# Optimization experiments

Measured on AMD Instinct MI355X. Metric: run time of the kernel, lower is better.

The kernel has to match this reference:

```python
import jax, jax.numpy as jnp
import numpy as np

B, F, T, K = 131072, 1024, 100, 32  # batch, num_features, num_trees, features per tree (sqrt(F))


def setup_inputs() -> dict:
    key = jax.random.key(0)
    kx, kw = jax.random.split(key)
    x = jax.random.normal(kx, (B, F), dtype=jnp.float32)
    # per-tree random feature selection without replacement (np.random.choice replace=False)
    rng = np.random.default_rng(0)
    idx = np.argsort(rng.random((T, F)), axis=1)[:, :K].astype(np.int32)
    feature_indices = jnp.asarray(idx)
    feature_thresholds = jnp.zeros((T, K), dtype=jnp.float32)  # lazy-init zeros in original
    feature_weights = jax.random.uniform(kw, (T, K), dtype=jnp.float32)  # torch.rand
    return {
        "x": x,
        "feature_indices": feature_indices,
        "feature_thresholds": feature_thresholds,
        "feature_weights": feature_weights,
    }


def reference(x, feature_indices, feature_thresholds, feature_weights):
    # Per tree t: ws_t = sum_k (x[:, idx[t,k]] - thr[t,k]) * w[t,k]
    # Equivalent fused form: scatter weights into a dense [T, F] matrix and do one GEMM,
    # with per-tree bias sum_k thr*w. scatter-add handles any duplicate indices identically
    # to the gather-then-sum formulation.
    T_, K_ = feature_indices.shape
    tree_ids = jnp.arange(T_, dtype=feature_indices.dtype)[:, None]  # [T,1]
    W_full = jnp.zeros((T_, x.shape[1]), dtype=x.dtype).at[tree_ids, feature_indices].add(feature_weights)
    bias = jnp.sum(feature_thresholds * feature_weights, axis=1)  # [T]
    ws = x @ W_full.T - bias[None, :]  # [B, T]
    p = jax.nn.sigmoid(ws)
    pm = jnp.mean(p, axis=1)  # mean over trees; mean(1-p) = 1 - mean(p)
    return jnp.stack([1.0 - pm, pm], axis=1)  # [B, 2]
```

## Files before the change

### kernel.cpp

```cpp
#include <hip/hip_runtime.h>
#include <math.h>

constexpr int Bn = 131072;
constexpr int Fn = 1024;
constexpr int Tn = 100;
constexpr int Kn = 32;

constexpr int BLOCK = 256;
constexpr int WPB   = BLOCK / 64;
constexpr int GRID  = 768;

using gptr_t = const __attribute__((address_space(1))) void*;
using lptr_t = __attribute__((address_space(3))) void*;

__global__ __launch_bounds__(BLOCK)
void rf_fwd(const float* __restrict__ x,
            const int*   __restrict__ fidx,
            const float* __restrict__ fthr,
            const float* __restrict__ fw,
            float*       __restrict__ out)
{
    __shared__ float ldsbuf[WPB][2][Fn];

    const int lane  = threadIdx.x & 63;
    const int wid   = threadIdx.x >> 6;
    const int gwave = blockIdx.x * WPB + wid;
    const int nwave = GRID * WPB;

    const int  t0   = lane;
    const bool has1 = (64 + lane) < Tn;
    const int  t1   = has1 ? (64 + lane) : lane;

    int   off0[Kn]; float w0[Kn];
    int   off1[Kn]; float w1[Kn];
    float bias0 = 0.f, bias1 = 0.f;

#pragma unroll
    for (int k = 0; k < Kn; k += 4) {
        int4   i4 = *(const int4*)  (fidx + t0 * Kn + k);
        float4 wv = *(const float4*)(fw   + t0 * Kn + k);
        float4 th = *(const float4*)(fthr + t0 * Kn + k);
        off0[k+0] = i4.x; off0[k+1] = i4.y; off0[k+2] = i4.z; off0[k+3] = i4.w;
        w0[k+0] = wv.x; w0[k+1] = wv.y; w0[k+2] = wv.z; w0[k+3] = wv.w;
        bias0 += th.x*wv.x + th.y*wv.y + th.z*wv.z + th.w*wv.w;
    }
#pragma unroll
    for (int k = 0; k < Kn; k += 4) {
        int4   i4 = *(const int4*)  (fidx + t1 * Kn + k);
        float4 wv = *(const float4*)(fw   + t1 * Kn + k);
        float4 th = *(const float4*)(fthr + t1 * Kn + k);
        off1[k+0] = i4.x; off1[k+1] = i4.y; off1[k+2] = i4.z; off1[k+3] = i4.w;
        w1[k+0] = wv.x; w1[k+1] = wv.y; w1[k+2] = wv.z; w1[k+3] = wv.w;
        bias1 += th.x*wv.x + th.y*wv.y + th.z*wv.z + th.w*wv.w;
    }

    float* buf0 = &ldsbuf[wid][0][0];
    float* buf1 = &ldsbuf[wid][1][0];

    auto stage = [&](const float* src, float* dst) {
#pragma unroll
        for (int c = 0; c < 4; ++c) {
            __builtin_amdgcn_global_load_lds(
                (gptr_t)(src + c * 256 + lane * 4),
                (lptr_t)(dst + c * 256),
                16, 0, 0);
        }
    };

    int row = gwave;
    if (row < Bn) stage(x + (size_t)row * Fn, buf0);

    float* cur = buf0;
    float* nxt = buf1;

    for (; row < Bn; row += nwave) {
        const int nrow = row + nwave;
        if (nrow < Bn) {
            stage(x + (size_t)nrow * Fn, nxt);
            asm volatile("s_waitcnt vmcnt(4)" ::: "memory");
        } else {
            asm volatile("s_waitcnt vmcnt(0)" ::: "memory");
        }

        float acc0 = 0.f, acc1 = 0.f;
#pragma unroll
        for (int k = 0; k < Kn; ++k) {
            acc0 = fmaf(cur[off0[k]], w0[k], acc0);
            acc1 = fmaf(cur[off1[k]], w1[k], acc1);
        }

        const float ws0 = acc0 - bias0;
        const float ws1 = acc1 - bias1;
        const float p0  = 1.f / (1.f + __expf(-ws0));
        const float p1  = 1.f / (1.f + __expf(-ws1));

        float s = p0 + (has1 ? p1 : 0.f);
#pragma unroll
        for (int d = 1; d < 64; d <<= 1) s += __shfl_xor(s, d, 64);

        if (lane == 0) {
            const float pm = s * (1.0f / Tn);
            *(float2*)(out + (size_t)row * 2) = make_float2(1.0f - pm, pm);
        }

        float* tmp = cur; cur = nxt; nxt = tmp;
    }
}

extern "C" void kernel_launch(void* const* d_in, const int* in_sizes, int n_in,
                              void* d_out, int out_size, void* d_ws, size_t ws_size,
                              hipStream_t stream) {
    const float* x    = (const float*)d_in[0];
    const int*   fidx = (const int*)  d_in[1];
    const float* fthr = (const float*)d_in[2];
    const float* fw   = (const float*)d_in[3];
    float*       out  = (float*)d_out;

    rf_fwd<<<GRID, BLOCK, 0, stream>>>(x, fidx, fthr, fw, out);
}
```

Before: 155.9 us.

## Replace sparse gather kernel with dense bf16 MFMA GEMM over scattered weights

Adds a prep kernel that scatters the per-tree weights into a dense, zero-padded bf16 [112 x 1024] matrix and computes the per-tree biases. The main kernel then streams x tiles into LDS and runs 16x16x32 bf16 MFMA instructions, with the sigmoid and mean over trees done in the epilogue. This is meant to replace the per-row LDS gathers with matrix-core work while still reading x once. It converts x and the weights to bf16, which loses precision, and it does roughly 32x more arithmetic than the sparse formulation.

```diff
diff --git a/kernel.cpp b/kernel.cpp
--- a/kernel.cpp
+++ b/kernel.cpp
@@ -6,104 +6,163 @@
 constexpr int Tn = 100;
 constexpr int Kn = 32;
 
+constexpr int TP = 112;
+constexpr int NF = TP / 16;
+constexpr int BK = 32;
+constexpr int NT = Fn / BK;
+constexpr int BM = 128;
+constexpr int MW = 32;
 constexpr int BLOCK = 256;
-constexpr int WPB   = BLOCK / 64;
-constexpr int GRID  = 768;
+constexpr int GRID = Bn / BM;
+
+typedef __attribute__((ext_vector_type(8))) short bf16x8;
+typedef __attribute__((ext_vector_type(4))) float f32x4;
 
 using gptr_t = const __attribute__((address_space(1))) void*;
 using lptr_t = __attribute__((address_space(3))) void*;
 
-__global__ __launch_bounds__(BLOCK)
-void rf_fwd(const float* __restrict__ x,
-            const int*   __restrict__ fidx,
-            const float* __restrict__ fthr,
-            const float* __restrict__ fw,
-            float*       __restrict__ out)
+__device__ inline unsigned short f2bf(float f) {
+    uint32_t u = __float_as_uint(f);
+    return (unsigned short)((u + 0x7FFFu + ((u >> 16) & 1u)) >> 16);
+}
+
+__global__ __launch_bounds__(64)
+void rf_prep(const int* __restrict__ fidx, const float* __restrict__ fthr,
+             const float* __restrict__ fw,
+             unsigned short* __restrict__ wt, float* __restrict__ bias)
 {
-    __shared__ float ldsbuf[WPB][2][Fn];
+    const int t    = blockIdx.x;
+    const int lane = threadIdx.x;
 
-    const int lane  = threadIdx.x & 63;
-    const int wid   = threadIdx.x >> 6;
-    const int gwave = blockIdx.x * WPB + wid;
-    const int nwave = GRID * WPB;
+    int4 z = make_int4(0, 0, 0, 0);
+    int4* rowp = (int4*)(wt + (size_t)t * Fn);
+    rowp[lane * 2 + 0] = z;
+    rowp[lane * 2 + 1] = z;
+    __syncthreads();
 
-    const int  t0   = lane;
-    const bool has1 = (64 + lane) < Tn;
-    const int  t1   = has1 ? (64 + lane) : lane;
-
-    int   off0[Kn]; float w0[Kn];
-    int   off1[Kn]; float w1[Kn];
-    float bias0 = 0.f, bias1 = 0.f;
-
-#pragma unroll
-    for (int k = 0; k < Kn; k += 4) {
-        int4   i4 = *(const int4*)  (fidx + t0 * Kn + k);
-        float4 wv = *(const float4*)(fw   + t0 * Kn + k);
-        float4 th = *(const float4*)(fthr + t0 * Kn + k);
-        off0[k+0] = i4.x; off0[k+1] = i4.y; off0[k+2] = i4.z; off0[k+3] = i4.w;
-        w0[k+0] = wv.x; w0[k+1] = wv.y; w0[k+2] = wv.z; w0[k+3] = wv.w;
-        bias0 += th.x*wv.x + th.y*wv.y + th.z*wv.z + th.w*wv.w;
+    float bsum = 0.f;
+    if (t < Tn && lane < Kn) {
+        const int   idx = fidx[t * Kn + lane];
+        const float w   = fw[t * Kn + lane];
+        const float th  = fthr[t * Kn + lane];
+        wt[(size_t)t * Fn + idx] = f2bf(w);
+        bsum = th * w;
     }
 #pragma unroll
-    for (int k = 0; k < Kn; k += 4) {
-        int4   i4 = *(const int4*)  (fidx + t1 * Kn + k);
-        float4 wv = *(const float4*)(fw   + t1 * Kn + k);
-        float4 th = *(const float4*)(fthr + t1 * Kn + k);
-        off1[k+0] = i4.x; off1[k+1] = i4.y; off1[k+2] = i4.z; off1[k+3] = i4.w;
-        w1[k+0] = wv.x; w1[k+1] = wv.y; w1[k+2] = wv.z; w1[k+3] = wv.w;
-        bias1 += th.x*wv.x + th.y*wv.y + th.z*wv.z + th.w*wv.w;
-    }
+    for (int d = 1; d < 64; d <<= 1) bsum += __shfl_xor(bsum, d, 64);
+    if (lane == 0) bias[t] = (t < Tn) ? bsum : 0.f;
+}
 
-    float* buf0 = &ldsbuf[wid][0][0];
-    float* buf1 = &ldsbuf[wid][1][0];
+__global__ __launch_bounds__(BLOCK)
+void rf_gemm(const float* __restrict__ x,
+             const unsigned short* __restrict__ wt,
+             const float* __restrict__ bias,
+             float* __restrict__ out)
+{
+    __shared__ float lds[2][BM * BK];
 
-    auto stage = [&](const float* src, float* dst) {
+    const int lane = threadIdx.x & 63;
+    const int wid  = threadIdx.x >> 6;
+    const int rb   = blockIdx.x * BM;
+
+    const int s_row = lane >> 3;
+    const int s_c16 = (lane & 7) ^ s_row;
+
+    const int a_rl  = lane & 15;
+    const int a_xor = lane & 7;
+    const int a_cb  = (lane >> 4) * 2;
+
+    f32x4 acc[2][NF];
 #pragma unroll
-        for (int c = 0; c < 4; ++c) {
-            __builtin_amdgcn_global_load_lds(
-                (gptr_t)(src + c * 256 + lane * 4),
-                (lptr_t)(dst + c * 256),
-                16, 0, 0);
+    for (int m = 0; m < 2; ++m)
+#pragma unroll
+        for (int f = 0; f < NF; ++f) acc[m][f] = (f32x4){0.f, 0.f, 0.f, 0.f};
+
+    auto stage = [&](int t, int bsel) {
+#pragma unroll
+        for (int i = 0; i < 4; ++i) {
+            const int win = wid * 4 + i;
+            const int row = win * 8 + s_row;
+            const float* src = x + (size_t)(rb + row) * Fn + t * BK + s_c16 * 4;
+            float* dst = &lds[bsel][win * 256];
+            __builtin_amdgcn_global_load_lds((gptr_t)src, (lptr_t)dst, 16, 0, 0);
         }
     };
 
-    int row = gwave;
-    if (row < Bn) stage(x + (size_t)row * Fn, buf0);
+    stage(0, 0);
+    __syncthreads();
 
-    float* cur = buf0;
-    float* nxt = buf1;
+    for (int t = 0; t < NT; ++t) {
+        const int cur = t & 1;
+        if (t + 1 < NT) stage(t + 1, cur ^ 1);
 
-    for (; row < Bn; row += nwave) {
-        const int nrow = row + nwave;
-        if (nrow < Bn) {
-            stage(x + (size_t)nrow * Fn, nxt);
-            asm volatile("s_waitcnt vmcnt(4)" ::: "memory");
-        } else {
-            asm volatile("s_waitcnt vmcnt(0)" ::: "memory");
+        bf16x8 bfr[NF];
+#pragma unroll
+        for (int f = 0; f < NF; ++f) {
+            const unsigned short* bp =
+                wt + (size_t)(f * 16 + a_rl) * Fn + t * BK + (lane >> 4) * 8;
+            bfr[f] = *(const bf16x8*)bp;
         }
 
-        float acc0 = 0.f, acc1 = 0.f;
+        const float* buf = lds[cur];
+        bf16x8 af[2];
 #pragma unroll
-        for (int k = 0; k < Kn; ++k) {
-            acc0 = fmaf(cur[off0[k]], w0[k], acc0);
-            acc1 = fmaf(cur[off1[k]], w1[k], acc1);
+        for (int m = 0; m < 2; ++m) {
+            const int row = wid * MW + m * 16 + a_rl;
+            const float* rp = buf + row * BK;
+            float4 lo = *(const float4*)(rp + (((a_cb + 0) ^ a_xor) * 4));
+            float4 hi = *(const float4*)(rp + (((a_cb + 1) ^ a_xor) * 4));
+            bf16x8 v;
+            v[0] = (short)f2bf(lo.x); v[1] = (short)f2bf(lo.y);
+            v[2] = (short)f2bf(lo.z); v[3] = (short)f2bf(lo.w);
+            v[4] = (short)f2bf(hi.x); v[5] = (short)f2bf(hi.y);
+            v[6] = (short)f2bf(hi.z); v[7] = (short)f2bf(hi.w);
+            af[m] = v;
         }
 
-        const float ws0 = acc0 - bias0;
-        const float ws1 = acc1 - bias1;
-        const float p0  = 1.f / (1.f + __expf(-ws0));
-        const float p1  = 1.f / (1.f + __expf(-ws1));
+#pragma unroll
+        for (int m = 0; m < 2; ++m)
+#pragma unroll
+            for (int f = 0; f < NF; ++f)
+                acc[m][f] = __builtin_amdgcn_mfma_f32_16x16x32_bf16(
+                    af[m], bfr[f], acc[m][f], 0, 0, 0);
 
-        float s = p0 + (has1 ? p1 : 0.f);
+        __syncthreads();
+    }
+
+    const int col = lane & 15;
+    float psum[2][4] = {};
 #pragma unroll
-        for (int d = 1; d < 64; d <<= 1) s += __shfl_xor(s, d, 64);
+    for (int f = 0; f < NF; ++f) {
+        const int  n     = f * 16 + col;
+        const bool valid = n < Tn;
+        const float bv   = bias[n];
+#pragma unroll
+        for (int m = 0; m < 2; ++m)
+#pragma unroll
+            for (int r = 0; r < 4; ++r) {
+                const float ws = acc[m][f][r] - bv;
+                const float p  = 1.f / (1.f + __expf(-ws));
+                if (valid) psum[m][r] += p;
+            }
+    }
+#pragma unroll
+    for (int m = 0; m < 2; ++m)
+#pragma unroll
+        for (int r = 0; r < 4; ++r)
+#pragma unroll
+            for (int d = 1; d < 16; d <<= 1)
+                psum[m][r] += __shfl_xor(psum[m][r], d, 64);
 
-        if (lane == 0) {
-            const float pm = s * (1.0f / Tn);
+    const int g = lane >> 4;
+#pragma unroll
+    for (int m = 0; m < 2; ++m) {
+        if (col < 4) {
+            const int r   = col;
+            const int row = rb + wid * MW + m * 16 + g * 4 + r;
+            const float pm = psum[m][r] * (1.0f / Tn);
             *(float2*)(out + (size_t)row * 2) = make_float2(1.0f - pm, pm);
         }
-
-        float* tmp = cur; cur = nxt; nxt = tmp;
     }
 }
 
@@ -116,5 +175,9 @@
     const float* fw   = (const float*)d_in[3];
     float*       out  = (float*)d_out;
 
-    rf_fwd<<<GRID, BLOCK, 0, stream>>>(x, fidx, fthr, fw, out);
+    unsigned short* wt   = (unsigned short*)d_ws;
+    float*          bias = (float*)((char*)d_ws + (size_t)TP * Fn * 2);
+
+    rf_prep<<<TP, 64, 0, stream>>>(fidx, fthr, fw, wt, bias);
+    rf_gemm<<<GRID, BLOCK, 0, stream>>>(x, wt, bias, out);
 }
```

Measured after the change: 168.3 us. 1.08x slower.
